# Optimization experiments

Measured on AMD Instinct MI355X. Metric: run time of the kernel, lower is better.

The kernel has to match this reference:

```python
import jax, jax.numpy as jnp
import numpy as np

D_MODEL = 1024
N_HEADS = 16
HEAD_DIM = 64
INNER = N_HEADS * HEAD_DIM  # 1024


def setup_inputs() -> dict:
    key = jax.random.key(0)
    ks = jax.random.split(key, 5)
    x = jax.random.normal(ks[0], (4, 2048, D_MODEL), dtype=jnp.float32)
    ln_w = jnp.ones((D_MODEL,), dtype=jnp.float32)
    ln_b = jnp.zeros((D_MODEL,), dtype=jnp.float32)
    w_qkv = jax.random.normal(ks[1], (D_MODEL, 3 * INNER), dtype=jnp.float32) * (D_MODEL ** -0.5)
    w_out = jax.random.normal(ks[2], (INNER, D_MODEL), dtype=jnp.float32) * (INNER ** -0.5)
    return {"x": x, "ln_w": ln_w, "ln_b": ln_b, "w_qkv": w_qkv, "w_out": w_out}


def reference(x, ln_w, ln_b, w_qkv, w_out):
    eps = 1e-5
    scale = HEAD_DIM ** -0.5
    # LayerNorm over last dim
    mu = jnp.mean(x, axis=-1, keepdims=True)
    var = jnp.mean(jnp.square(x - mu), axis=-1, keepdims=True)
    h = (x - mu) * jax.lax.rsqrt(var + eps) * ln_w + ln_b
    # QKV projection: [b, n, 3*inner]
    qkv = h @ w_qkv
    q, k, v = jnp.split(qkv, 3, axis=-1)
    b, n, _ = q.shape
    def heads(t):
        return t.reshape(b, n, N_HEADS, HEAD_DIM).transpose(0, 2, 1, 3)  # b h n d
    q, k, v = heads(q), heads(k), heads(v)
    dots = jnp.einsum('bhnd,bhmd->bhnm', q, k) * scale  # [b,h,n,n]
    attn = jax.nn.softmax(dots, axis=-1)
    out = jnp.einsum('bhnm,bhmd->bhnd', attn, v)
    out = out.transpose(0, 2, 1, 3).reshape(b, n, INNER)
    return out @ w_out
```

## Files before the change

### kernel.cpp

```cpp
#include <hip/hip_runtime.h>
#include <hip/hip_bf16.h>

typedef __bf16 bf16x8 __attribute__((ext_vector_type(8)));
typedef float f32x4 __attribute__((ext_vector_type(4)));
typedef short s16x4 __attribute__((ext_vector_type(4)));

#define D_MODEL 1024
#define N_SEQ   2048
#define N_BATCH 4
#define N_HEADS 16
#define HEAD_DIM 64
#define M_ROWS  (N_BATCH * N_SEQ)
#define N_QKV   (3 * D_MODEL)

__device__ __forceinline__ void async_copy16(const void* g, void* s) {
    __builtin_amdgcn_global_load_lds(
        (const __attribute__((address_space(1))) unsigned*)g,
        (__attribute__((address_space(3))) unsigned*)s, 16, 0, 0);
}

__global__ __launch_bounds__(256) void ln_kernel(
    const float* __restrict__ x, const float* __restrict__ w,
    const float* __restrict__ b, __hip_bfloat16* __restrict__ h)
{
    __shared__ float red[8];
    long row = blockIdx.x;
    int tid = threadIdx.x;
    float4 xv = *(const float4*)&x[row * D_MODEL + tid * 4];
    float s = xv.x + xv.y + xv.z + xv.w;
    #pragma unroll
    for (int o = 32; o; o >>= 1) s += __shfl_down(s, o);
    if ((tid & 63) == 0) red[tid >> 6] = s;
    __syncthreads();
    float mu = (red[0] + red[1] + red[2] + red[3]) * (1.f / 1024.f);
    float d0 = xv.x - mu, d1 = xv.y - mu, d2 = xv.z - mu, d3 = xv.w - mu;
    float vs = d0 * d0 + d1 * d1 + d2 * d2 + d3 * d3;
    #pragma unroll
    for (int o = 32; o; o >>= 1) vs += __shfl_down(vs, o);
    if ((tid & 63) == 0) red[4 + (tid >> 6)] = vs;
    __syncthreads();
    float var = (red[4] + red[5] + red[6] + red[7]) * (1.f / 1024.f);
    float inv = rsqrtf(var + 1e-5f);
    float4 wv = *(const float4*)&w[tid * 4];
    float4 bv = *(const float4*)&b[tid * 4];
    union { ushort4 u; __hip_bfloat16 h[4]; } o4;
    o4.h[0] = __float2bfloat16(d0 * inv * wv.x + bv.x);
    o4.h[1] = __float2bfloat16(d1 * inv * wv.y + bv.y);
    o4.h[2] = __float2bfloat16(d2 * inv * wv.z + bv.z);
    o4.h[3] = __float2bfloat16(d3 * inv * wv.w + bv.w);
    *(ushort4*)&h[row * D_MODEL + tid * 4] = o4.u;
}

__global__ __launch_bounds__(256) void transpose_cast(
    const float* __restrict__ src, __hip_bfloat16* __restrict__ dst, int R, int C)
{
    __shared__ float tile[32][33];
    int tx = threadIdx.x, ty = threadIdx.y;
    int c0 = blockIdx.x * 32, r0 = blockIdx.y * 32;
    #pragma unroll
    for (int j = 0; j < 32; j += 8)
        tile[ty + j][tx] = src[(long)(r0 + ty + j) * C + c0 + tx];
    __syncthreads();
    #pragma unroll
    for (int j = 0; j < 32; j += 8)
        dst[(long)(c0 + ty + j) * R + r0 + tx] = __float2bfloat16(tile[tx][ty + j]);
}

__global__ __launch_bounds__(256) void gemm_bt(
    const __hip_bfloat16* __restrict__ A, const __hip_bfloat16* __restrict__ Bt,
    int M, int Nn, int K, int mode,
    __hip_bfloat16* __restrict__ qb, __hip_bfloat16* __restrict__ kb,
    __hip_bfloat16* __restrict__ vbt, float* __restrict__ outp)
{
    __shared__ __hip_bfloat16 As[128 * 32];
    __shared__ __hip_bfloat16 Bs[128 * 32];
    int tid = threadIdx.x;
    int wave = tid >> 6, lane = tid & 63, quad = lane >> 4, l15 = lane & 15;
    int wm = (wave >> 1) * 64, wn = (wave & 1) * 64;
    long bm = blockIdx.y, bn = blockIdx.x;

    f32x4 acc[4][4] = {};

    for (int k0 = 0; k0 < K; k0 += 32) {
        __syncthreads();
        #pragma unroll
        for (int s = 0; s < 2; ++s) {
            int seg = tid + s * 256;
            int row = seg >> 2, c8 = (seg & 3) * 8;
            async_copy16(&A[(bm * 128 + row) * K + k0 + c8], &As[seg * 8]);
            async_copy16(&Bt[(bn * 128 + row) * K + k0 + c8], &Bs[seg * 8]);
        }
        __syncthreads();
        bf16x8 af[4], bfr[4];
        #pragma unroll
        for (int t = 0; t < 4; ++t) {
            af[t]  = *(const bf16x8*)&As[(wm + t * 16 + l15) * 32 + quad * 8];
            bfr[t] = *(const bf16x8*)&Bs[(wn + t * 16 + l15) * 32 + quad * 8];
        }
        #pragma unroll
        for (int tm = 0; tm < 4; ++tm)
            #pragma unroll
            for (int tn = 0; tn < 4; ++tn)
                acc[tm][tn] = __builtin_amdgcn_mfma_f32_16x16x32_bf16(
                    af[tm], bfr[tn], acc[tm][tn], 0, 0, 0);
    }

    if (mode == 0) {
        #pragma unroll
        for (int tm = 0; tm < 4; ++tm)
            #pragma unroll
            for (int tn = 0; tn < 4; ++tn)
                #pragma unroll
                for (int r = 0; r < 4; ++r) {
                    long row = bm * 128 + wm + tm * 16 + quad * 4 + r;
                    long col = bn * 128 + wn + tn * 16 + l15;
                    outp[row * Nn + col] = acc[tm][tn][r];
                }
    } else {
        #pragma unroll
        for (int tm = 0; tm < 4; ++tm)
            #pragma unroll
            for (int tn = 0; tn < 4; ++tn)
                #pragma unroll
                for (int r = 0; r < 4; ++r) {
                    long row = bm * 128 + wm + tm * 16 + quad * 4 + r;
                    int col = (int)(bn * 128) + wn + tn * 16 + l15;
                    int which = col >> 10;
                    int inner = col & 1023;
                    int head = inner >> 6;
                    int d = inner & 63;
                    long bb = row >> 11;
                    long n = row & 2047;
                    __hip_bfloat16 val = __float2bfloat16(acc[tm][tn][r]);
                    if (which == 2) {
                        long idx = (((bb * N_HEADS + head) * HEAD_DIM) + d) * N_SEQ + n;
                        vbt[idx] = val;
                    } else {
                        long idx = (((bb * N_HEADS + head) * N_SEQ) + n) * HEAD_DIM + d;
                        if (which == 0) qb[idx] = val;
                        else kb[idx] = val;
                    }
                }
    }
}

__global__ __launch_bounds__(256) void attn_kernel(
    const __hip_bfloat16* __restrict__ q, const __hip_bfloat16* __restrict__ k,
    const __hip_bfloat16* __restrict__ vt, __hip_bfloat16* __restrict__ ao)
{
    __shared__ __hip_bfloat16 Ks[64][68];
    __shared__ __hip_bfloat16 Vs[64][68];
    int tid = threadIdx.x;
    int wave = tid >> 6, lane = tid & 63, quad = lane >> 4, l15 = lane & 15;
    int bh = blockIdx.y;
    int q0 = blockIdx.x * 128;
    const long base = (long)bh * N_SEQ * HEAD_DIM;
    const float cs2 = 0.125f * 1.44269504f;

    bf16x8 qf[2][2];
    #pragma unroll
    for (int qs = 0; qs < 2; ++qs)
        #pragma unroll
        for (int hh = 0; hh < 2; ++hh)
            qf[qs][hh] = *(const bf16x8*)&q[base
                + (long)(q0 + wave * 32 + qs * 16 + l15) * HEAD_DIM
                + hh * 32 + quad * 8];

    f32x4 Oacc[2][4] = {};
    float l_run[2] = { 0.f, 0.f };
    union PFrag { s16x4 v; __hip_bfloat16 h[4]; };
    PFrag pfr[2][4];

    for (int kt = 0; kt < N_SEQ / 64; ++kt) {
        int key0 = kt * 64;
        __syncthreads();
        #pragma unroll
        for (int s = 0; s < 2; ++s) {
            int seg = tid + s * 256;
            int r = seg >> 3, c8 = (seg & 7) * 8;
            *(uint4*)&Ks[r][c8] =
                *(const uint4*)&k[base + (long)(key0 + r) * HEAD_DIM + c8];
            *(uint4*)&Vs[r][c8] =
                *(const uint4*)&vt[base + (long)r * N_SEQ + key0 + c8];
        }
        __syncthreads();

        bf16x8 kf[4][2];
        #pragma unroll
        for (int tk = 0; tk < 4; ++tk)
            #pragma unroll
            for (int hh = 0; hh < 2; ++hh)
                kf[tk][hh] = *(const bf16x8*)&Ks[tk * 16 + l15][hh * 32 + quad * 8];

        #pragma unroll
        for (int qs = 0; qs < 2; ++qs) {
            #pragma unroll
            for (int tk = 0; tk < 4; ++tk) {
                f32x4 a = {};
                a = __builtin_amdgcn_mfma_f32_16x16x32_bf16(kf[tk][0], qf[qs][0], a, 0, 0, 0);
                a = __builtin_amdgcn_mfma_f32_16x16x32_bf16(kf[tk][1], qf[qs][1], a, 0, 0, 0);
                float rs = 0.f;
                #pragma unroll
                for (int r = 0; r < 4; ++r) {
                    float pv = exp2f(a[r] * cs2);
                    pfr[qs][tk].h[r] = __float2bfloat16(pv);
                    rs += pv;
                }
                l_run[qs] += rs;
            }
        }

        #pragma unroll
        for (int dt = 0; dt < 4; ++dt) {
            s16x4 vf[4];
            #pragma unroll
            for (int tk = 0; tk < 4; ++tk)
                vf[tk] = *(const s16x4*)&Vs[dt * 16 + l15][tk * 16 + quad * 4];
            #pragma unroll
            for (int qs = 0; qs < 2; ++qs)
                #pragma unroll
                for (int tk = 0; tk < 4; ++tk)
                    Oacc[qs][dt] = __builtin_amdgcn_mfma_f32_16x16x16bf16_1k(
                        pfr[qs][tk].v, vf[tk], Oacc[qs][dt], 0, 0, 0);
        }
    }

    int b = bh >> 4, h = bh & 15;
    #pragma unroll
    for (int qs = 0; qs < 2; ++qs) {
        float ltot = l_run[qs];
        ltot += __shfl_xor(ltot, 16);
        ltot += __shfl_xor(ltot, 32);
        float linv[4];
        #pragma unroll
        for (int r = 0; r < 4; ++r)
            linv[r] = 1.f / __shfl(ltot, quad * 4 + r);
        #pragma unroll
        for (int dt = 0; dt < 4; ++dt)
            #pragma unroll
            for (int r = 0; r < 4; ++r) {
                int n = q0 + wave * 32 + qs * 16 + quad * 4 + r;
                ao[((long)(b * N_SEQ + n)) * D_MODEL + h * HEAD_DIM + dt * 16 + l15] =
                    __float2bfloat16(Oacc[qs][dt][r] * linv[r]);
            }
    }
}

extern "C" void kernel_launch(void* const* d_in, const int* in_sizes, int n_in,
                              void* d_out, int out_size, void* d_ws, size_t ws_size,
                              hipStream_t stream)
{
    const float* x     = (const float*)d_in[0];
    const float* ln_w  = (const float*)d_in[1];
    const float* ln_b  = (const float*)d_in[2];
    const float* w_qkv = (const float*)d_in[3];
    const float* w_out = (const float*)d_in[4];
    float* out = (float*)d_out;

    char* ws = (char*)d_ws;
    __hip_bfloat16* h_bf   = (__hip_bfloat16*)(ws);
    __hip_bfloat16* wqkv_t = (__hip_bfloat16*)(ws + 16777216);
    __hip_bfloat16* wout_t = (__hip_bfloat16*)(ws + 23068672);
    __hip_bfloat16* qb     = (__hip_bfloat16*)(ws + 25165824);
    __hip_bfloat16* kb     = (__hip_bfloat16*)(ws + 41943040);
    __hip_bfloat16* vbt    = (__hip_bfloat16*)(ws + 58720256);
    __hip_bfloat16* ao     = (__hip_bfloat16*)(ws + 75497472);

    ln_kernel<<<M_ROWS, 256, 0, stream>>>(x, ln_w, ln_b, h_bf);
    transpose_cast<<<dim3(N_QKV / 32, D_MODEL / 32), dim3(32, 8), 0, stream>>>(
        w_qkv, wqkv_t, D_MODEL, N_QKV);
    transpose_cast<<<dim3(D_MODEL / 32, D_MODEL / 32), dim3(32, 8), 0, stream>>>(
        w_out, wout_t, D_MODEL, D_MODEL);
    gemm_bt<<<dim3(N_QKV / 128, M_ROWS / 128), 256, 0, stream>>>(
        h_bf, wqkv_t, M_ROWS, N_QKV, D_MODEL, 1, qb, kb, vbt, nullptr);
    attn_kernel<<<dim3(N_SEQ / 128, N_BATCH * N_HEADS), 256, 0, stream>>>(qb, kb, vbt, ao);
    gemm_bt<<<dim3(D_MODEL / 128, M_ROWS / 128), 256, 0, stream>>>(
        ao, wout_t, M_ROWS, D_MODEL, D_MODEL, 0, nullptr, nullptr, nullptr, out);
}
```

Measured before the change: 389.9 us.

## Stage QKV epilogue through LDS for vectorized stores, prefetch K/V, fold scale

```diff
diff --git a/kernel.cpp b/kernel.cpp
--- a/kernel.cpp
+++ b/kernel.cpp
@@ -12,6 +12,7 @@
 #define HEAD_DIM 64
 #define M_ROWS  (N_BATCH * N_SEQ)
 #define N_QKV   (3 * D_MODEL)
+#define CS2     0.18033688f
 
 __device__ __forceinline__ void async_copy16(const void* g, void* s) {
     __builtin_amdgcn_global_load_lds(
@@ -72,12 +73,14 @@
     __hip_bfloat16* __restrict__ qb, __hip_bfloat16* __restrict__ kb,
     __hip_bfloat16* __restrict__ vbt, float* __restrict__ outp)
 {
-    __shared__ __hip_bfloat16 As[128 * 32];
-    __shared__ __hip_bfloat16 Bs[128 * 32];
+    __shared__ __hip_bfloat16 smem[128 * 136];
+    __hip_bfloat16* As = smem;
+    __hip_bfloat16* Bs = smem + 4096;
     int tid = threadIdx.x;
     int wave = tid >> 6, lane = tid & 63, quad = lane >> 4, l15 = lane & 15;
     int wm = (wave >> 1) * 64, wn = (wave & 1) * 64;
     long bm = blockIdx.y, bn = blockIdx.x;
+    bool swapop = (mode == 1) && (bn < 16);
 
     f32x4 acc[4][4] = {};
 
@@ -97,12 +100,21 @@
             af[t]  = *(const bf16x8*)&As[(wm + t * 16 + l15) * 32 + quad * 8];
             bfr[t] = *(const bf16x8*)&Bs[(wn + t * 16 + l15) * 32 + quad * 8];
         }
-        #pragma unroll
-        for (int tm = 0; tm < 4; ++tm)
-            #pragma unroll
-            for (int tn = 0; tn < 4; ++tn)
-                acc[tm][tn] = __builtin_amdgcn_mfma_f32_16x16x32_bf16(
-                    af[tm], bfr[tn], acc[tm][tn], 0, 0, 0);
+        if (swapop) {
+            #pragma unroll
+            for (int tm = 0; tm < 4; ++tm)
+                #pragma unroll
+                for (int tn = 0; tn < 4; ++tn)
+                    acc[tm][tn] = __builtin_amdgcn_mfma_f32_16x16x32_bf16(
+                        bfr[tn], af[tm], acc[tm][tn], 0, 0, 0);
+        } else {
+            #pragma unroll
+            for (int tm = 0; tm < 4; ++tm)
+                #pragma unroll
+                for (int tn = 0; tn < 4; ++tn)
+                    acc[tm][tn] = __builtin_amdgcn_mfma_f32_16x16x32_bf16(
+                        af[tm], bfr[tn], acc[tm][tn], 0, 0, 0);
+        }
     }
 
     if (mode == 0) {
@@ -116,31 +128,59 @@
                     long col = bn * 128 + wn + tn * 16 + l15;
                     outp[row * Nn + col] = acc[tm][tn][r];
                 }
+        return;
+    }
+
+    int which = (int)(bn >> 3);
+    __syncthreads();
+    if (which < 2) {
+        float esc = (which == 0) ? CS2 : 1.0f;
+        #pragma unroll
+        for (int tm = 0; tm < 4; ++tm)
+            #pragma unroll
+            for (int tn = 0; tn < 4; ++tn) {
+                union { ushort4 u; __hip_bfloat16 h[4]; } pk;
+                #pragma unroll
+                for (int r = 0; r < 4; ++r)
+                    pk.h[r] = __float2bfloat16(acc[tm][tn][r] * esc);
+                *(ushort4*)&smem[(wm + tm * 16 + l15) * 136 + wn + tn * 16 + quad * 4] = pk.u;
+            }
+        __syncthreads();
+        __hip_bfloat16* ptr = (which == 0) ? qb : kb;
+        #pragma unroll
+        for (int it = 0; it < 8; ++it) {
+            int idx = it * 256 + tid;
+            int lr = idx >> 4, lc = (idx & 15) * 8;
+            uint4 vv = *(const uint4*)&smem[lr * 136 + lc];
+            long row = bm * 128 + lr;
+            long bb = row >> 11, n = row & 2047;
+            int cg = (int)bn * 128 + lc - which * 1024;
+            int head = cg >> 6, d = cg & 63;
+            *(uint4*)&ptr[(((bb * 16 + head) * 2048) + n) * 64 + d] = vv;
+        }
     } else {
         #pragma unroll
         for (int tm = 0; tm < 4; ++tm)
             #pragma unroll
-            for (int tn = 0; tn < 4; ++tn)
-                #pragma unroll
-                for (int r = 0; r < 4; ++r) {
-                    long row = bm * 128 + wm + tm * 16 + quad * 4 + r;
-                    int col = (int)(bn * 128) + wn + tn * 16 + l15;
-                    int which = col >> 10;
-                    int inner = col & 1023;
-                    int head = inner >> 6;
-                    int d = inner & 63;
-                    long bb = row >> 11;
-                    long n = row & 2047;
-                    __hip_bfloat16 val = __float2bfloat16(acc[tm][tn][r]);
-                    if (which == 2) {
-                        long idx = (((bb * N_HEADS + head) * HEAD_DIM) + d) * N_SEQ + n;
-                        vbt[idx] = val;
-                    } else {
-                        long idx = (((bb * N_HEADS + head) * N_SEQ) + n) * HEAD_DIM + d;
-                        if (which == 0) qb[idx] = val;
-                        else kb[idx] = val;
-                    }
-                }
+            for (int tn = 0; tn < 4; ++tn) {
+                union { ushort4 u; __hip_bfloat16 h[4]; } pk;
+                #pragma unroll
+                for (int r = 0; r < 4; ++r)
+                    pk.h[r] = __float2bfloat16(acc[tm][tn][r]);
+                *(ushort4*)&smem[(wn + tn * 16 + l15) * 136 + wm + tm * 16 + quad * 4] = pk.u;
+            }
+        __syncthreads();
+        #pragma unroll
+        for (int it = 0; it < 8; ++it) {
+            int idx = it * 256 + tid;
+            int lr = idx >> 4, lc = (idx & 15) * 8;
+            uint4 vv = *(const uint4*)&smem[lr * 136 + lc];
+            int cg = (int)bn * 128 + lr - 2048;
+            int head = cg >> 6, d = cg & 63;
+            long nrow = bm * 128 + lc;
+            long bb = nrow >> 11, n = nrow & 2047;
+            *(uint4*)&vbt[((bb * 16 + head) * 64 + d) * 2048 + n] = vv;
+        }
     }
 }
 
@@ -155,7 +195,6 @@
     int bh = blockIdx.y;
     int q0 = blockIdx.x * 128;
     const long base = (long)bh * N_SEQ * HEAD_DIM;
-    const float cs2 = 0.125f * 1.44269504f;
 
     bf16x8 qf[2][2];
     #pragma unroll
@@ -171,19 +210,36 @@
     union PFrag { s16x4 v; __hip_bfloat16 h[4]; };
     PFrag pfr[2][4];
 
+    int sr[2], sc[2];
+    #pragma unroll
+    for (int s = 0; s < 2; ++s) {
+        int seg = tid + s * 256;
+        sr[s] = seg >> 3; sc[s] = (seg & 7) * 8;
+    }
+
+    uint4 kpre[2], vpre[2];
+    #pragma unroll
+    for (int s = 0; s < 2; ++s) {
+        kpre[s] = *(const uint4*)&k[base + (long)sr[s] * HEAD_DIM + sc[s]];
+        vpre[s] = *(const uint4*)&vt[base + (long)sr[s] * N_SEQ + sc[s]];
+    }
+
     for (int kt = 0; kt < N_SEQ / 64; ++kt) {
-        int key0 = kt * 64;
         __syncthreads();
         #pragma unroll
         for (int s = 0; s < 2; ++s) {
-            int seg = tid + s * 256;
-            int r = seg >> 3, c8 = (seg & 7) * 8;
-            *(uint4*)&Ks[r][c8] =
-                *(const uint4*)&k[base + (long)(key0 + r) * HEAD_DIM + c8];
-            *(uint4*)&Vs[r][c8] =
-                *(const uint4*)&vt[base + (long)r * N_SEQ + key0 + c8];
-        }
-        __syncthreads();
+            *(uint4*)&Ks[sr[s]][sc[s]] = kpre[s];
+            *(uint4*)&Vs[sr[s]][sc[s]] = vpre[s];
+        }
+        __syncthreads();
+        if (kt + 1 < N_SEQ / 64) {
+            int key1 = (kt + 1) * 64;
+            #pragma unroll
+            for (int s = 0; s < 2; ++s) {
+                kpre[s] = *(const uint4*)&k[base + (long)(key1 + sr[s]) * HEAD_DIM + sc[s]];
+                vpre[s] = *(const uint4*)&vt[base + (long)sr[s] * N_SEQ + key1 + sc[s]];
+            }
+        }
 
         bf16x8 kf[4][2];
         #pragma unroll
@@ -202,7 +258,7 @@
                 float rs = 0.f;
                 #pragma unroll
                 for (int r = 0; r < 4; ++r) {
-                    float pv = exp2f(a[r] * cs2);
+                    float pv = exp2f(a[r]);
                     pfr[qs][tk].h[r] = __float2bfloat16(pv);
                     rs += pv;
                 }
@@ -221,7 +277,7 @@
                 #pragma unroll
                 for (int tk = 0; tk < 4; ++tk)
                     Oacc[qs][dt] = __builtin_amdgcn_mfma_f32_16x16x16bf16_1k(
-                        pfr[qs][tk].v, vf[tk], Oacc[qs][dt], 0, 0, 0);
+                        vf[tk], pfr[qs][tk].v, Oacc[qs][dt], 0, 0, 0);
         }
     }
 
@@ -231,18 +287,17 @@
         float ltot = l_run[qs];
         ltot += __shfl_xor(ltot, 16);
         ltot += __shfl_xor(ltot, 32);
-        float linv[4];
-        #pragma unroll
-        for (int r = 0; r < 4; ++r)
-            linv[r] = 1.f / __shfl(ltot, quad * 4 + r);
-        #pragma unroll
-        for (int dt = 0; dt < 4; ++dt)
-            #pragma unroll
-            for (int r = 0; r < 4; ++r) {
-                int n = q0 + wave * 32 + qs * 16 + quad * 4 + r;
-                ao[((long)(b * N_SEQ + n)) * D_MODEL + h * HEAD_DIM + dt * 16 + l15] =
-                    __float2bfloat16(Oacc[qs][dt][r] * linv[r]);
-            }
+        float linv = 1.f / ltot;
+        int n = q0 + wave * 32 + qs * 16 + l15;
+        #pragma unroll
+        for (int dt = 0; dt < 4; ++dt) {
+            union { ushort4 u; __hip_bfloat16 h[4]; } pk;
+            #pragma unroll
+            for (int r = 0; r < 4; ++r)
+                pk.h[r] = __float2bfloat16(Oacc[qs][dt][r] * linv);
+            *(ushort4*)&ao[((long)(b * N_SEQ + n)) * D_MODEL
+                           + h * HEAD_DIM + dt * 16 + quad * 4] = pk.u;
+        }
     }
 }
 
```

New measurement: 480.0 us. 23.1% more time.
